# Performance work log

Measured on AMD Instinct MI355X. Metric: run time of the kernel, lower is better.

The kernel has to match this reference:

```python
import jax, jax.numpy as jnp
import numpy as np

SCALE = 10000.0
EPS = 1e-5


def _extract_patches(x):
    # x: [B,28,28] int32 -> [B,28,28,9] (3x3 neighborhoods, zero-padded)
    xp = jnp.pad(x, ((0, 0), (1, 1), (1, 1)))
    ps = [xp[:, i:i + 28, j:j + 28] for i in range(3) for j in range(3)]
    return jnp.stack(ps, axis=-1)


def _bn_eval(x, g, b, m, v):
    inv = g / jnp.sqrt(v + EPS)
    return x * inv[None, :, None, None] + (b - m * inv)[None, :, None, None]


def _maxpool2(x):
    return jax.lax.reduce_window(x, -jnp.inf, jax.lax.max,
                                 (1, 1, 2, 2), (1, 1, 2, 2), 'VALID')


def _conv(x, w, b):
    y = jax.lax.conv_general_dilated(x, w, (1, 1), 'SAME',
                                     dimension_numbers=('NCHW', 'OIHW', 'NCHW'))
    return y + b[None, :, None, None]


def setup_inputs() -> dict:
    key = jax.random.key(0)
    ks = jax.random.split(key, 24)
    B = 1024
    inp = {}
    inp['x_img'] = jax.random.randint(ks[0], (B, 28, 28), 0, 256, dtype=jnp.int32)
    # quantized conv1 weights: round(w * 10000), signed
    inp['y_int'] = jax.random.randint(ks[1], (16, 9), 0, 20001, dtype=jnp.int32) - 10000
    inp['bias1'] = jax.random.normal(ks[2], (16,), jnp.float32)
    for i, (c, kg, kb, km, kv) in enumerate([(16, 3, 4, 5, 6), (32, 7, 8, 9, 10), (64, 11, 12, 13, 14)]):
        j = i + 1
        inp[f'g{j}'] = jax.random.uniform(ks[kg], (c,), jnp.float32, 0.5, 1.5)
        inp[f'b{j}'] = jax.random.normal(ks[kb], (c,), jnp.float32)
        inp[f'm{j}'] = jax.random.normal(ks[km], (c,), jnp.float32)
        inp[f'v{j}'] = jax.random.uniform(ks[kv], (c,), jnp.float32, 0.5, 1.5)
    inp['w2'] = jax.random.normal(ks[15], (32, 16, 3, 3), jnp.float32) * 0.1
    inp['bias2'] = jax.random.normal(ks[16], (32,), jnp.float32)
    inp['w3'] = jax.random.normal(ks[17], (64, 32, 3, 3), jnp.float32) * 0.1
    inp['bias3'] = jax.random.normal(ks[18], (64,), jnp.float32)
    inp['w_fc1'] = jax.random.normal(ks[19], (128, 576), jnp.float32) * 0.05
    inp['b_fc1'] = jax.random.normal(ks[20], (128,), jnp.float32)
    inp['w_fc2'] = jax.random.normal(ks[21], (10, 128), jnp.float32) * 0.1
    inp['b_fc2'] = jax.random.normal(ks[22], (10,), jnp.float32)
    return inp


def reference(x_img, y_int, bias1, g1, b1, m1, v1, w2, bias2, g2, b2, m2, v2,
              w3, bias3, g3, b3, m3, v3, w_fc1, b_fc1, w_fc2, b_fc2):
    # IPFE first conv: exact integer inner product <patch, y>, then /10000 + bias
    patches = _extract_patches(x_img)                      # [B,28,28,9] int32
    ip = jnp.einsum('bhwk,ok->bohw', patches, y_int)       # exact int32 dot
    feat = ip.astype(jnp.float32) / SCALE + bias1[None, :, None, None]  # [B,16,28,28]
    feat = _maxpool2(jax.nn.relu(_bn_eval(feat, g1, b1, m1, v1)))       # [B,16,14,14]
    feat = _maxpool2(jax.nn.relu(_bn_eval(_conv(feat, w2, bias2), g2, b2, m2, v2)))  # [B,32,7,7]
    feat = _maxpool2(jax.nn.relu(_bn_eval(_conv(feat, w3, bias3), g3, b3, m3, v3)))  # [B,64,3,3]
    flat = feat.reshape(feat.shape[0], -1)                 # [B,576]
    h = jax.nn.relu(flat @ w_fc1.T + b_fc1)                # [B,128] (dropout: eval mode)
    return h @ w_fc2.T + b_fc2                             # [B,10]
```

## Files before the change

kernel.cpp:

```cpp
#include <hip/hip_runtime.h>
#include <hip/hip_bf16.h>

#define EPS 1e-5f

typedef __attribute__((ext_vector_type(8))) short bf16x8;
typedef __attribute__((ext_vector_type(4))) float f32x4;
typedef unsigned short ushort_t;
#define MFMA16(a, b, c) __builtin_amdgcn_mfma_f32_16x16x32_bf16(a, b, c, 0, 0, 0)

#define CST_OFF  144
#define W2F_H    1024
#define W3F_H    6144
#define WFC1F_H  24576
#define PREP_ITEMS (368 + 5120 + 18432 + 73728)

__device__ __forceinline__ unsigned short f2bf(float f) {
    unsigned int u = __builtin_bit_cast(unsigned int, f);
    return (unsigned short)((u + 0x7fffu + ((u >> 16) & 1u)) >> 16);
}

__global__ __launch_bounds__(256) void prep_kernel(
    const int* __restrict__ y_int,
    const float* __restrict__ w2, const float* __restrict__ w3,
    const float* __restrict__ wfc1,
    const float* __restrict__ bias1,
    const float* __restrict__ g1, const float* __restrict__ b1,
    const float* __restrict__ m1, const float* __restrict__ v1,
    const float* __restrict__ g2, const float* __restrict__ b2,
    const float* __restrict__ m2, const float* __restrict__ v2,
    const float* __restrict__ bias2,
    const float* __restrict__ g3, const float* __restrict__ b3,
    const float* __restrict__ m3, const float* __restrict__ v3,
    const float* __restrict__ bias3,
    float* __restrict__ ws)
{
    unsigned short* wsh = (unsigned short*)ws;
    int i = blockIdx.x * 256 + threadIdx.x;
    if (i < 144) {
        int k = i >> 4, c = i & 15;
        ws[i] = (float)y_int[c * 9 + k];
    } else if (i < 368) {
        int idx = i - 144;
        if (idx < 16) { int c = idx;
            ws[CST_OFF + idx] = g1[c] * rsqrtf(v1[c] + EPS) * 1e-4f;
        } else if (idx < 32) { int c = idx - 16;
            float inv = g1[c] * rsqrtf(v1[c] + EPS);
            ws[CST_OFF + idx] = bias1[c] * inv + b1[c] - m1[c] * inv;
        } else if (idx < 64) { int c = idx - 32;
            ws[CST_OFF + idx] = g2[c] * rsqrtf(v2[c] + EPS);
        } else if (idx < 96) { int c = idx - 64;
            float inv = g2[c] * rsqrtf(v2[c] + EPS);
            ws[CST_OFF + idx] = bias2[c] * inv + b2[c] - m2[c] * inv;
        } else if (idx < 160) { int c = idx - 96;
            ws[CST_OFF + idx] = g3[c] * rsqrtf(v3[c] + EPS);
        } else { int c = idx - 160;
            float inv = g3[c] * rsqrtf(v3[c] + EPS);
            ws[CST_OFF + idx] = bias3[c] * inv + b3[c] - m3[c] * inv;
        }
    } else {
        int e = i - 368;
        if (e < 5120) {
            int m = e / 2560, r = e % 2560, s = r >> 9, l = (r >> 3) & 63, j = e & 7;
            int kl  = ((l >> 4) << 3) + j;
            int tap = 2 * s + (kl >> 4), ci = kl & 15;
            int ch  = m * 16 + (l & 15);
            float v = (tap < 9) ? w2[ch * 144 + ci * 9 + tap] : 0.f;
            wsh[W2F_H + e] = f2bf(v);
        } else if (e < 5120 + 18432) {
            int e3 = e - 5120;
            int mt = e3 / 4608, r = e3 % 4608, ks = r >> 9, l = (r >> 3) & 63, j = e3 & 7;
            int ch = mt * 16 + (l & 15), ci = ((l >> 4) << 3) + j;
            wsh[W3F_H + e3] = f2bf(w3[ch * 288 + ci * 9 + ks]);
        } else {
            int ef = e - 23552;
            int mt = ef / 9216, r = ef % 9216, ks = r >> 9, l = (r >> 3) & 63, j = ef & 7;
            int ch = mt * 16 + (l & 15), k = ks * 32 + ((l >> 4) << 3) + j;
            wsh[WFC1F_H + ef] = f2bf(wfc1[ch * 576 + k]);
        }
    }
}

__global__ __launch_bounds__(256, 4) void fused_cnn(
    const int* __restrict__ x_img,
    const float* __restrict__ ws,
    const float* __restrict__ bfc1,
    const float* __restrict__ wfc2, const float* __restrict__ bfc2,
    float* __restrict__ out)
{
    const int tid  = threadIdx.x;
    const int lane = tid & 63;
    const int wv   = __builtin_amdgcn_readfirstlane(tid >> 6);
    const int img  = blockIdx.x;
    const unsigned short* wsh = (const unsigned short*)ws;

    __shared__ __align__(16) float s_img[900];
    __shared__ __align__(16) char  s_f1[8192];
    __shared__ __align__(16) char  s_f2[5184];
    ushort_t* FLAT = (ushort_t*)s_f1;
    float*    H    = (float*)(s_f1 + 1152);

    const int* xp = x_img + img * 784;
    for (int i = tid; i < 900; i += 256) {
        int r = i / 30, c = i - r * 30;
        float v = 0.f;
        if (r >= 1 && r <= 28 && c >= 1 && c <= 28)
            v = (float)xp[(r - 1) * 28 + (c - 1)];
        s_img[i] = v;
    }
    {
        uint4 z = make_uint4(0u, 0u, 0u, 0u);
        for (int i = tid; i < 512; i += 256) ((uint4*)s_f1)[i] = z;
        for (int i = tid; i < 324; i += 256) ((uint4*)s_f2)[i] = z;
    }
    __syncthreads();

    if (tid < 196) {
        int ph = tid / 14, pw = tid - (tid / 14) * 14;
        float acc[16][4];
        #pragma unroll
        for (int c = 0; c < 16; c++) {
            acc[c][0] = 0.f; acc[c][1] = 0.f; acc[c][2] = 0.f; acc[c][3] = 0.f;
        }
        const float* imgq = s_img + ph * 60 + pw * 2;
        #pragma unroll
        for (int k = 0; k < 9; k++) {
            const float* ip = imgq + (k / 3) * 30 + (k % 3);
            float x0 = ip[0], x1 = ip[1], x2 = ip[30], x3 = ip[31];
            const float4* yw = (const float4*)(ws + k * 16);
            float4 wA = yw[0], wB = yw[1], wC = yw[2], wD = yw[3];
            float wr[16] = {wA.x, wA.y, wA.z, wA.w, wB.x, wB.y, wB.z, wB.w,
                            wC.x, wC.y, wC.z, wC.w, wD.x, wD.y, wD.z, wD.w};
            #pragma unroll
            for (int c = 0; c < 16; c++) {
                float w = wr[c];
                acc[c][0] += w * x0; acc[c][1] += w * x1;
                acc[c][2] += w * x2; acc[c][3] += w * x3;
            }
        }
        unsigned int pk[8];
        #pragma unroll
        for (int c = 0; c < 16; c += 2) {
            float mx0 = fmaxf(fmaxf(acc[c][0], acc[c][1]), fmaxf(acc[c][2], acc[c][3]));
            float r0  = fmaxf(mx0 * ws[CST_OFF + c] + ws[CST_OFF + 16 + c], 0.f);
            float mx1 = fmaxf(fmaxf(acc[c+1][0], acc[c+1][1]), fmaxf(acc[c+1][2], acc[c+1][3]));
            float r1  = fmaxf(mx1 * ws[CST_OFF + c + 1] + ws[CST_OFF + 16 + c + 1], 0.f);
            pk[c >> 1] = (unsigned int)f2bf(r0) | ((unsigned int)f2bf(r1) << 16);
        }
        int pos = (ph + 1) * 16 + (pw + 1);
        *(uint4*)(s_f1 + pos * 16)        = make_uint4(pk[0], pk[1], pk[2], pk[3]);
        *(uint4*)(s_f1 + 4096 + pos * 16) = make_uint4(pk[4], pk[5], pk[6], pk[7]);
    }
    __syncthreads();

    {
        const int x = lane & 15, g = lane >> 4;
        const int t = g >> 1, c0 = g & 1;
        bf16x8 A2[2][5];
        #pragma unroll
        for (int m = 0; m < 2; m++)
            #pragma unroll
            for (int s = 0; s < 5; s++)
                A2[m][s] = *(const bf16x8*)(const void*)(wsh + W2F_H + ((m * 5 + s) * 64 + lane) * 8);
        int voff[5];
        #pragma unroll
        for (int s = 0; s < 5; s++) {
            int tap = 2 * s + t;
            int dy = (tap < 9) ? tap / 3 : 0, dx = (tap < 9) ? tap % 3 : 0;
            voff[s] = c0 * 4096 + (dy * 16 + x + dx) * 16;
        }
        float a2v[2][4], c2v[2][4];
        #pragma unroll
        for (int m = 0; m < 2; m++)
            #pragma unroll
            for (int r = 0; r < 4; r++) {
                int ch = m * 16 + g * 4 + r;
                a2v[m][r] = ws[CST_OFF + 32 + ch];
                c2v[m][r] = ws[CST_OFF + 64 + ch];
            }
        for (int p = wv; p < 7; p += 4) {
            const char* bp = s_f1 + p * 512;
            bf16x8 B0[5], B1[5];
            #pragma unroll
            for (int s = 0; s < 5; s++) {
                B0[s] = *(const bf16x8*)(const void*)(bp + voff[s]);
                B1[s] = *(const bf16x8*)(const void*)(bp + 256 + voff[s]);
            }
            #pragma unroll
            for (int m = 0; m < 2; m++) {
                f32x4 a0 = {0.f, 0.f, 0.f, 0.f}, a1 = {0.f, 0.f, 0.f, 0.f};
                #pragma unroll
                for (int s = 0; s < 5; s++) {
                    a0 = MFMA16(A2[m][s], B0[s], a0);
                    a1 = MFMA16(A2[m][s], B1[s], a1);
                }
                float hp[4];
                #pragma unroll
                for (int r = 0; r < 4; r++) {
                    float vp = fmaxf(a0[r], a1[r]);
                    hp[r] = fmaxf(vp, __shfl_xor(vp, 1));
                }
                if (!(x & 1) && x < 14) {
                    int xp2 = x >> 1;
                    int pp  = (p + 1) * 9 + xp2 + 1;
                    int ch0 = m * 16 + g * 4;
                    unsigned int lo = (unsigned int)f2bf(fmaxf(hp[0] * a2v[m][0] + c2v[m][0], 0.f)) |
                                      ((unsigned int)f2bf(fmaxf(hp[1] * a2v[m][1] + c2v[m][1], 0.f)) << 16);
                    unsigned int hi = (unsigned int)f2bf(fmaxf(hp[2] * a2v[m][2] + c2v[m][2], 0.f)) |
                                      ((unsigned int)f2bf(fmaxf(hp[3] * a2v[m][3] + c2v[m][3], 0.f)) << 16);
                    *(uint2*)(s_f2 + (ch0 >> 3) * 1296 + pp * 16 + (ch0 & 7) * 2) = make_uint2(lo, hi);
                }
            }
        }
    }
    __syncthreads();

    {
        const int mt = wv;
        bf16x8 A3[9];
        #pragma unroll
        for (int ks = 0; ks < 9; ks++)
            A3[ks] = *(const bf16x8*)(const void*)(wsh + W3F_H + ((mt * 9 + ks) * 64 + lane) * 8);
        const int x8 = lane & 7, ry = (lane >> 3) & 1, qg = lane >> 4;
        int voff3[9];
        #pragma unroll
        for (int ks = 0; ks < 9; ks++) {
            int dy = ks / 3, dx = ks % 3;
            voff3[ks] = qg * 1296 + ((ry + dy) * 9 + x8 + dx) * 16;
        }
        float a3v[4], c3v[4];
        #pragma unroll
        for (int r = 0; r < 4; r++) {
            int ch = mt * 16 + qg * 4 + r;
            a3v[r] = ws[CST_OFF + 96 + ch];
            c3v[r] = ws[CST_OFF + 160 + ch];
        }
        #pragma unroll
        for (int t = 0; t < 3; t++) {
            bf16x8 bb[9];
            #pragma unroll
            for (int ks = 0; ks < 9; ks++)
                bb[ks] = *(const bf16x8*)(const void*)(s_f2 + t * 288 + voff3[ks]);
            f32x4 acc = {0.f, 0.f, 0.f, 0.f};
            #pragma unroll
            for (int ks = 0; ks < 9; ks++)
                acc = MFMA16(A3[ks], bb[ks], acc);
            float hp[4];
            #pragma unroll
            for (int r = 0; r < 4; r++) {
                float vp = fmaxf(acc[r], __shfl_xor(acc[r], 8));
                hp[r] = fmaxf(vp, __shfl_xor(vp, 1));
            }
            if (ry == 0 && !(x8 & 1) && x8 < 6) {
                int xp3 = x8 >> 1;
                int ch0 = mt * 16 + qg * 4;
                #pragma unroll
                for (int r = 0; r < 4; r++) {
                    float v = fmaxf(hp[r] * a3v[r] + c3v[r], 0.f);
                    FLAT[(ch0 + r) * 9 + t * 3 + xp3] = f2bf(v);
                }
            }
        }
    }
    __syncthreads();

    {
        const int g = lane >> 4;
        bf16x8 BB[18];
        #pragma unroll
        for (int ks = 0; ks < 18; ks++)
            BB[ks] = *(const bf16x8*)(const void*)(FLAT + ks * 32 + g * 8);
        #pragma unroll
        for (int mi = 0; mi < 2; mi++) {
            int mt = wv + mi * 4;
            f32x4 acc = {0.f, 0.f, 0.f, 0.f};
            #pragma unroll
            for (int ks = 0; ks < 18; ks++) {
                bf16x8 a = *(const bf16x8*)(const void*)(wsh + WFC1F_H + ((mt * 18 + ks) * 64 + lane) * 8);
                acc = MFMA16(a, BB[ks], acc);
            }
            if ((lane & 15) == 0) {
                int ch0 = mt * 16 + g * 4;
                #pragma unroll
                for (int r = 0; r < 4; r++)
                    H[ch0 + r] = fmaxf(acc[r] + bfc1[ch0 + r], 0.f);
            }
        }
    }
    __syncthreads();

    if (tid < 160) {
        int o = tid / 16, l = tid & 15;
        float a = 0.f;
        #pragma unroll
        for (int k = l; k < 128; k += 16)
            a += H[k] * wfc2[o * 128 + k];
        a += __shfl_xor(a, 8);
        a += __shfl_xor(a, 4);
        a += __shfl_xor(a, 2);
        a += __shfl_xor(a, 1);
        if (l == 0) out[img * 10 + o] = a + bfc2[o];
    }
}

extern "C" void kernel_launch(void* const* d_in, const int* in_sizes, int n_in,
                              void* d_out, int out_size, void* d_ws, size_t ws_size,
                              hipStream_t stream) {
    float* ws = (float*)d_ws;
    prep_kernel<<<(PREP_ITEMS + 255) / 256, 256, 0, stream>>>(
        (const int*)d_in[1],
        (const float*)d_in[15],
        (const float*)d_in[17],
        (const float*)d_in[19],
        (const float*)d_in[2],
        (const float*)d_in[3], (const float*)d_in[4], (const float*)d_in[5], (const float*)d_in[6],
        (const float*)d_in[7], (const float*)d_in[8], (const float*)d_in[9], (const float*)d_in[10],
        (const float*)d_in[16],
        (const float*)d_in[11], (const float*)d_in[12], (const float*)d_in[13], (const float*)d_in[14],
        (const float*)d_in[18],
        ws);
    fused_cnn<<<1024, 256, 0, stream>>>(
        (const int*)d_in[0],
        ws,
        (const float*)d_in[20],
        (const float*)d_in[21], (const float*)d_in[22],
        (float*)d_out);
}
```

Before: 27.42 us.

## Split per-image pipeline into three independent wave slices with halo recompute

Each block now uses three waves, and each wave owns one output row of the 3x3 conv3 map. The wave recomputes the halo rows of conv1 and conv2 it needs in private LDS, which removes the block-wide barriers between stages. FC1 is split by K across waves into partial sums that are reduced after one barrier. The fc1 weight prep is permuted to match the new position-major flatten. This trades redundant conv1/conv2 halo work and reloading all conv3 weights per wave for fewer syncs and more independent wave progress.

Result: slower. 45.45 us (+65.8%).

```diff
diff --git a/kernel.cpp b/kernel.cpp
--- a/kernel.cpp
+++ b/kernel.cpp
@@ -74,13 +74,15 @@
         } else {
             int ef = e - 23552;
             int mt = ef / 9216, r = ef % 9216, ks = r >> 9, l = (r >> 3) & 63, j = ef & 7;
-            int ch = mt * 16 + (l & 15), k = ks * 32 + ((l >> 4) << 3) + j;
-            wsh[WFC1F_H + ef] = f2bf(wfc1[ch * 576 + k]);
+            int ch = mt * 16 + (l & 15);
+            int kp = ks * 32 + ((l >> 4) << 3) + j;
+            int ci = kp & 63, pos = kp >> 6;
+            wsh[WFC1F_H + ef] = f2bf(wfc1[ch * 576 + ci * 9 + pos]);
         }
     }
 }
 
-__global__ __launch_bounds__(256, 4) void fused_cnn(
+__global__ __launch_bounds__(192, 3) void fused_cnn(
     const int* __restrict__ x_img,
     const float* __restrict__ ws,
     const float* __restrict__ bfc1,
@@ -93,35 +95,43 @@
     const int img  = blockIdx.x;
     const unsigned short* wsh = (const unsigned short*)ws;
 
-    __shared__ __align__(16) float s_img[900];
-    __shared__ __align__(16) char  s_f1[8192];
-    __shared__ __align__(16) char  s_f2[5184];
-    ushort_t* FLAT = (ushort_t*)s_f1;
-    float*    H    = (float*)(s_f1 + 1152);
-
-    const int* xp = x_img + img * 784;
-    for (int i = tid; i < 900; i += 256) {
-        int r = i / 30, c = i - r * 30;
-        float v = 0.f;
-        if (r >= 1 && r <= 28 && c >= 1 && c <= 28)
-            v = (float)xp[(r - 1) * 28 + (c - 1)];
-        s_img[i] = v;
-    }
+    __shared__ __align__(16) char s_all[32928];
+    char*     W    = s_all + wv * 10080;
+    float*    IMG  = (float*)W;
+    char*     F1w  = W + 2640;
+    char*     F2w  = W + 7760;
+    ushort_t* FLAT = (ushort_t*)(s_all + 30240);
+    float*    Hp   = (float*)(s_all + 31392);
+
+    const int F0  = (wv == 0) ? 0 : (wv == 1) ? 2 : 6;
+    const int I0  = (wv == 0) ? 0 : (wv == 1) ? 2 : 10;
+    const int PR0 = (wv == 0) ? 0 : (wv == 1) ? 1 : 5;
+    const int NQ  = (wv == 0) ? 98 : (wv == 1) ? 140 : 126;
+    const int PX0 = (wv == 0) ? 0 : (wv == 1) ? 1 : 9;
+    const int NPX = (wv == 0) ? 15 : (wv == 1) ? 22 : 19;
+    const int PS  = (wv == 0) ? 0 : (wv == 1) ? 1 : 3;
+    const int PC  = (wv == 0) ? 3 : 4;
+    const int LR0 = (wv == 0) ? -1 : (wv == 1) ? 1 : 3;
+
     {
         uint4 z = make_uint4(0u, 0u, 0u, 0u);
-        for (int i = tid; i < 512; i += 256) ((uint4*)s_f1)[i] = z;
-        for (int i = tid; i < 324; i += 256) ((uint4*)s_f2)[i] = z;
-    }
-    __syncthreads();
-
-    if (tid < 196) {
-        int ph = tid / 14, pw = tid - (tid / 14) * 14;
+        uint4* zp = (uint4*)W;
+        for (int j = lane; j < 630; j += 64) zp[j] = z;
+    }
+    const int* xp = x_img + img * 784;
+    for (int j = lane; j < NPX * 28; j += 64) {
+        int rr = j / 28, cc = j - rr * 28;
+        IMG[(PX0 + rr + 1 - I0) * 30 + 1 + cc] = (float)xp[(PX0 + rr) * 28 + cc];
+    }
+
+    for (int q = lane; q < NQ; q += 64) {
+        int pr = PR0 + q / 14, pw = q % 14;
         float acc[16][4];
         #pragma unroll
         for (int c = 0; c < 16; c++) {
             acc[c][0] = 0.f; acc[c][1] = 0.f; acc[c][2] = 0.f; acc[c][3] = 0.f;
         }
-        const float* imgq = s_img + ph * 60 + pw * 2;
+        const float* imgq = IMG + (2 * pr - I0) * 30 + pw * 2;
         #pragma unroll
         for (int k = 0; k < 9; k++) {
             const float* ip = imgq + (k / 3) * 30 + (k % 3);
@@ -146,15 +156,14 @@
             float r1  = fmaxf(mx1 * ws[CST_OFF + c + 1] + ws[CST_OFF + 16 + c + 1], 0.f);
             pk[c >> 1] = (unsigned int)f2bf(r0) | ((unsigned int)f2bf(r1) << 16);
         }
-        int pos = (ph + 1) * 16 + (pw + 1);
-        *(uint4*)(s_f1 + pos * 16)        = make_uint4(pk[0], pk[1], pk[2], pk[3]);
-        *(uint4*)(s_f1 + 4096 + pos * 16) = make_uint4(pk[4], pk[5], pk[6], pk[7]);
-    }
-    __syncthreads();
+        int L = pr + 1 - F0;
+        *(uint4*)(F1w + L * 256 + (pw + 1) * 16)        = make_uint4(pk[0], pk[1], pk[2], pk[3]);
+        *(uint4*)(F1w + 2560 + L * 256 + (pw + 1) * 16) = make_uint4(pk[4], pk[5], pk[6], pk[7]);
+    }
 
     {
         const int x = lane & 15, g = lane >> 4;
-        const int t = g >> 1, c0 = g & 1;
+        const int t2 = g >> 1, c0 = g & 1;
         bf16x8 A2[2][5];
         #pragma unroll
         for (int m = 0; m < 2; m++)
@@ -164,9 +173,9 @@
         int voff[5];
         #pragma unroll
         for (int s = 0; s < 5; s++) {
-            int tap = 2 * s + t;
+            int tap = 2 * s + t2;
             int dy = (tap < 9) ? tap / 3 : 0, dx = (tap < 9) ? tap % 3 : 0;
-            voff[s] = c0 * 4096 + (dy * 16 + x + dx) * 16;
+            voff[s] = c0 * 2560 + (dy * 16 + x + dx) * 16;
         }
         float a2v[2][4], c2v[2][4];
         #pragma unroll
@@ -177,8 +186,9 @@
                 a2v[m][r] = ws[CST_OFF + 32 + ch];
                 c2v[m][r] = ws[CST_OFF + 64 + ch];
             }
-        for (int p = wv; p < 7; p += 4) {
-            const char* bp = s_f1 + p * 512;
+        for (int i = 0; i < PC; i++) {
+            int p = PS + i;
+            const char* bp = F1w + (2 * p - F0) * 256;
             bf16x8 B0[5], B1[5];
             #pragma unroll
             for (int s = 0; s < 5; s++) {
@@ -201,45 +211,32 @@
                 }
                 if (!(x & 1) && x < 14) {
                     int xp2 = x >> 1;
-                    int pp  = (p + 1) * 9 + xp2 + 1;
+                    int lrow = p - LR0;
                     int ch0 = m * 16 + g * 4;
                     unsigned int lo = (unsigned int)f2bf(fmaxf(hp[0] * a2v[m][0] + c2v[m][0], 0.f)) |
                                       ((unsigned int)f2bf(fmaxf(hp[1] * a2v[m][1] + c2v[m][1], 0.f)) << 16);
                     unsigned int hi = (unsigned int)f2bf(fmaxf(hp[2] * a2v[m][2] + c2v[m][2], 0.f)) |
                                       ((unsigned int)f2bf(fmaxf(hp[3] * a2v[m][3] + c2v[m][3], 0.f)) << 16);
-                    *(uint2*)(s_f2 + (ch0 >> 3) * 1296 + pp * 16 + (ch0 & 7) * 2) = make_uint2(lo, hi);
+                    *(uint2*)(F2w + (ch0 >> 3) * 576 + (lrow * 9 + xp2 + 1) * 16 + (ch0 & 7) * 2) = make_uint2(lo, hi);
                 }
             }
         }
     }
-    __syncthreads();
 
     {
-        const int mt = wv;
-        bf16x8 A3[9];
-        #pragma unroll
-        for (int ks = 0; ks < 9; ks++)
-            A3[ks] = *(const bf16x8*)(const void*)(wsh + W3F_H + ((mt * 9 + ks) * 64 + lane) * 8);
         const int x8 = lane & 7, ry = (lane >> 3) & 1, qg = lane >> 4;
-        int voff3[9];
+        bf16x8 bb[9];
         #pragma unroll
         for (int ks = 0; ks < 9; ks++) {
             int dy = ks / 3, dx = ks % 3;
-            voff3[ks] = qg * 1296 + ((ry + dy) * 9 + x8 + dx) * 16;
-        }
-        float a3v[4], c3v[4];
-        #pragma unroll
-        for (int r = 0; r < 4; r++) {
-            int ch = mt * 16 + qg * 4 + r;
-            a3v[r] = ws[CST_OFF + 96 + ch];
-            c3v[r] = ws[CST_OFF + 160 + ch];
-        }
-        #pragma unroll
-        for (int t = 0; t < 3; t++) {
-            bf16x8 bb[9];
+            bb[ks] = *(const bf16x8*)(const void*)(F2w + qg * 576 + ((ry + dy) * 9 + x8 + dx) * 16);
+        }
+        #pragma unroll
+        for (int mt = 0; mt < 4; mt++) {
+            bf16x8 A3[9];
             #pragma unroll
             for (int ks = 0; ks < 9; ks++)
-                bb[ks] = *(const bf16x8*)(const void*)(s_f2 + t * 288 + voff3[ks]);
+                A3[ks] = *(const bf16x8*)(const void*)(wsh + W3F_H + ((mt * 9 + ks) * 64 + lane) * 8);
             f32x4 acc = {0.f, 0.f, 0.f, 0.f};
             #pragma unroll
             for (int ks = 0; ks < 9; ks++)
@@ -255,50 +252,55 @@
                 int ch0 = mt * 16 + qg * 4;
                 #pragma unroll
                 for (int r = 0; r < 4; r++) {
-                    float v = fmaxf(hp[r] * a3v[r] + c3v[r], 0.f);
-                    FLAT[(ch0 + r) * 9 + t * 3 + xp3] = f2bf(v);
+                    float a3 = ws[CST_OFF + 96 + ch0 + r];
+                    float c3 = ws[CST_OFF + 160 + ch0 + r];
+                    float v = fmaxf(hp[r] * a3 + c3, 0.f);
+                    FLAT[(wv * 3 + xp3) * 64 + ch0 + r] = f2bf(v);
                 }
             }
         }
     }
-    __syncthreads();
 
     {
         const int g = lane >> 4;
-        bf16x8 BB[18];
-        #pragma unroll
-        for (int ks = 0; ks < 18; ks++)
-            BB[ks] = *(const bf16x8*)(const void*)(FLAT + ks * 32 + g * 8);
-        #pragma unroll
-        for (int mi = 0; mi < 2; mi++) {
-            int mt = wv + mi * 4;
-            f32x4 acc = {0.f, 0.f, 0.f, 0.f};
-            #pragma unroll
-            for (int ks = 0; ks < 18; ks++) {
-                bf16x8 a = *(const bf16x8*)(const void*)(wsh + WFC1F_H + ((mt * 18 + ks) * 64 + lane) * 8);
-                acc = MFMA16(a, BB[ks], acc);
-            }
-            if ((lane & 15) == 0) {
-                int ch0 = mt * 16 + g * 4;
+        f32x4 acc8[8];
+        #pragma unroll
+        for (int mt = 0; mt < 8; mt++) acc8[mt] = (f32x4){0.f, 0.f, 0.f, 0.f};
+        #pragma unroll
+        for (int mt = 0; mt < 8; mt++) {
+            #pragma unroll
+            for (int ksl = 0; ksl < 6; ksl++) {
+                int ks = wv * 6 + ksl;
+                bf16x8 a  = *(const bf16x8*)(const void*)(wsh + WFC1F_H + ((mt * 18 + ks) * 64 + lane) * 8);
+                bf16x8 bv = *(const bf16x8*)(const void*)(FLAT + ks * 32 + g * 8);
+                acc8[mt] = MFMA16(a, bv, acc8[mt]);
+            }
+        }
+        if ((lane & 15) == 0) {
+            #pragma unroll
+            for (int mt = 0; mt < 8; mt++)
                 #pragma unroll
                 for (int r = 0; r < 4; r++)
-                    H[ch0 + r] = fmaxf(acc[r] + bfc1[ch0 + r], 0.f);
-            }
+                    Hp[wv * 128 + mt * 16 + g * 4 + r] = acc8[mt][r];
         }
     }
     __syncthreads();
 
-    if (tid < 160) {
-        int o = tid / 16, l = tid & 15;
-        float a = 0.f;
-        #pragma unroll
-        for (int k = l; k < 128; k += 16)
-            a += H[k] * wfc2[o * 128 + k];
-        a += __shfl_xor(a, 8);
-        a += __shfl_xor(a, 4);
-        a += __shfl_xor(a, 2);
-        a += __shfl_xor(a, 1);
-        if (l == 0) out[img * 10 + o] = a + bfc2[o];
+    if (wv == 0) {
+        int ch = lane * 2;
+        float h0 = fmaxf(Hp[ch]     + Hp[128 + ch]     + Hp[256 + ch]     + bfc1[ch],     0.f);
+        float h1 = fmaxf(Hp[ch + 1] + Hp[128 + ch + 1] + Hp[256 + ch + 1] + bfc1[ch + 1], 0.f);
+        #pragma unroll
+        for (int o = 0; o < 10; o++) {
+            float a = wfc2[o * 128 + ch] * h0 + wfc2[o * 128 + ch + 1] * h1;
+            a += __shfl_xor(a, 32);
+            a += __shfl_xor(a, 16);
+            a += __shfl_xor(a, 8);
+            a += __shfl_xor(a, 4);
+            a += __shfl_xor(a, 2);
+            a += __shfl_xor(a, 1);
+            if (lane == 0) out[img * 10 + o] = a + bfc2[o];
+        }
     }
 }
 
@@ -318,7 +320,7 @@
         (const float*)d_in[11], (const float*)d_in[12], (const float*)d_in[13], (const float*)d_in[14],
         (const float*)d_in[18],
         ws);
-    fused_cnn<<<1024, 256, 0, stream>>>(
+    fused_cnn<<<1024, 192, 0, stream>>>(
         (const int*)d_in[0],
         ws,
         (const float*)d_in[20],
```

## Split FC1 by K per wave, load image directly, zero only borders

Applied to the files above, without the earlier changes.

Each wave now does FC1 on its own conv3 output-channel slice (K split) instead of waiting for all of FLAT, which removes one block-wide barrier. The per-wave partial sums are combined along with bias and ReLU in the FC2 stage. The FC1 weight layout is padded to 160 entries per wave slice, and conv1 reads its 4x4 pixel neighbourhoods straight from global memory instead of a padded shared image. This drops the s_img stage and another barrier. Only the halo borders of the shared feature buffers are zeroed now, at the cost of more FC1 weight traffic and redundant global pixel loads.

Measured after the change: 27.22 us (median of 2 runs). No clear change (-0.7%).

```diff
diff --git a/kernel.cpp b/kernel.cpp
--- a/kernel.cpp
+++ b/kernel.cpp
@@ -12,7 +12,7 @@
 #define W2F_H    1024
 #define W3F_H    6144
 #define WFC1F_H  24576
-#define PREP_ITEMS (368 + 5120 + 18432 + 73728)
+#define PREP_ITEMS (368 + 5120 + 18432 + 81920)
 
 __device__ __forceinline__ unsigned short f2bf(float f) {
     unsigned int u = __builtin_bit_cast(unsigned int, f);
@@ -73,9 +73,14 @@
             wsh[W3F_H + e3] = f2bf(w3[ch * 288 + ci * 9 + ks]);
         } else {
             int ef = e - 23552;
-            int mt = ef / 9216, r = ef % 9216, ks = r >> 9, l = (r >> 3) & 63, j = ef & 7;
-            int ch = mt * 16 + (l & 15), k = ks * 32 + ((l >> 4) << 3) + j;
-            wsh[WFC1F_H + ef] = f2bf(wfc1[ch * 576 + k]);
+            int mt = ef / 10240, r = ef % 10240;
+            int ks = r >> 9, l = (r >> 3) & 63, j = ef & 7;
+            int ch = mt * 16 + (l & 15);
+            int kp = ks * 32 + ((l >> 4) << 3) + j;
+            int w  = kp / 160, lk = kp - w * 160;
+            float v = 0.f;
+            if (lk < 144) v = wfc1[ch * 576 + (w * 16 + lk / 9) * 9 + (lk % 9)];
+            wsh[WFC1F_H + ef] = f2bf(v);
         }
     }
 }
@@ -93,39 +98,59 @@
     const int img  = blockIdx.x;
     const unsigned short* wsh = (const unsigned short*)ws;
 
-    __shared__ __align__(16) float s_img[900];
-    __shared__ __align__(16) char  s_f1[8192];
-    __shared__ __align__(16) char  s_f2[5184];
+    __shared__ __align__(16) char s_f1[8192];
+    __shared__ __align__(16) char s_f2[5184];
     ushort_t* FLAT = (ushort_t*)s_f1;
-    float*    H    = (float*)(s_f1 + 1152);
-
-    const int* xp = x_img + img * 784;
-    for (int i = tid; i < 900; i += 256) {
-        int r = i / 30, c = i - r * 30;
-        float v = 0.f;
-        if (r >= 1 && r <= 28 && c >= 1 && c <= 28)
-            v = (float)xp[(r - 1) * 28 + (c - 1)];
-        s_img[i] = v;
-    }
+    float*    Hp   = (float*)(s_f1 + 1536);
+
     {
         uint4 z = make_uint4(0u, 0u, 0u, 0u);
-        for (int i = tid; i < 512; i += 256) ((uint4*)s_f1)[i] = z;
-        for (int i = tid; i < 324; i += 256) ((uint4*)s_f2)[i] = z;
-    }
-    __syncthreads();
+        if (tid < 120) {
+            int c0 = tid / 60, b = tid % 60, pos;
+            if (b < 16)      pos = b;
+            else if (b < 32) pos = 240 + (b - 16);
+            else if (b < 46) pos = (b - 31) * 16;
+            else             pos = (b - 45) * 16 + 15;
+            *(uint4*)(s_f1 + c0 * 4096 + pos * 16) = z;
+        } else if (tid < 248) {
+            int zz = tid - 120;
+            int q = zz / 32, b = zz % 32, pos;
+            if (b < 9)       pos = b;
+            else if (b < 18) pos = 72 + (b - 9);
+            else if (b < 25) pos = (b - 17) * 9;
+            else             pos = (b - 24) * 9 + 8;
+            *(uint4*)(s_f2 + q * 1296 + pos * 16) = z;
+        }
+    }
 
     if (tid < 196) {
         int ph = tid / 14, pw = tid - (tid / 14) * 14;
+        const int* xp = x_img + img * 784;
+        int ry0 = 2 * ph - 1, cx0 = 2 * pw - 1;
+        float px[4][4];
+        #pragma unroll
+        for (int dy = 0; dy < 4; dy++) {
+            int ry = ry0 + dy;
+            int ryc = min(max(ry, 0), 27);
+            bool rok = (unsigned)ry < 28u;
+            #pragma unroll
+            for (int dx = 0; dx < 4; dx++) {
+                int cx = cx0 + dx;
+                int cxc = min(max(cx, 0), 27);
+                float v = (float)xp[ryc * 28 + cxc];
+                px[dy][dx] = (rok && (unsigned)cx < 28u) ? v : 0.f;
+            }
+        }
         float acc[16][4];
         #pragma unroll
         for (int c = 0; c < 16; c++) {
             acc[c][0] = 0.f; acc[c][1] = 0.f; acc[c][2] = 0.f; acc[c][3] = 0.f;
         }
-        const float* imgq = s_img + ph * 60 + pw * 2;
         #pragma unroll
         for (int k = 0; k < 9; k++) {
-            const float* ip = imgq + (k / 3) * 30 + (k % 3);
-            float x0 = ip[0], x1 = ip[1], x2 = ip[30], x3 = ip[31];
+            int ty = k / 3, tx = k % 3;
+            float x0 = px[ty][tx],     x1 = px[ty][tx + 1];
+            float x2 = px[ty + 1][tx], x3 = px[ty + 1][tx + 1];
             const float4* yw = (const float4*)(ws + k * 16);
             float4 wA = yw[0], wB = yw[1], wC = yw[2], wD = yw[3];
             float wr[16] = {wA.x, wA.y, wA.z, wA.w, wB.x, wB.y, wB.z, wB.w,
@@ -154,7 +179,7 @@
 
     {
         const int x = lane & 15, g = lane >> 4;
-        const int t = g >> 1, c0 = g & 1;
+        const int t2 = g >> 1, c0 = g & 1;
         bf16x8 A2[2][5];
         #pragma unroll
         for (int m = 0; m < 2; m++)
@@ -164,7 +189,7 @@
         int voff[5];
         #pragma unroll
         for (int s = 0; s < 5; s++) {
-            int tap = 2 * s + t;
+            int tap = 2 * s + t2;
             int dy = (tap < 9) ? tap / 3 : 0, dx = (tap < 9) ? tap % 3 : 0;
             voff[s] = c0 * 4096 + (dy * 16 + x + dx) * 16;
         }
@@ -234,6 +259,7 @@
             a3v[r] = ws[CST_OFF + 96 + ch];
             c3v[r] = ws[CST_OFF + 160 + ch];
         }
+        if (lane < 16) FLAT[wv * 160 + 144 + lane] = 0;
         #pragma unroll
         for (int t = 0; t < 3; t++) {
             bf16x8 bb[9];
@@ -252,37 +278,33 @@
             }
             if (ry == 0 && !(x8 & 1) && x8 < 6) {
                 int xp3 = x8 >> 1;
-                int ch0 = mt * 16 + qg * 4;
                 #pragma unroll
                 for (int r = 0; r < 4; r++) {
                     float v = fmaxf(hp[r] * a3v[r] + c3v[r], 0.f);
-                    FLAT[(ch0 + r) * 9 + t * 3 + xp3] = f2bf(v);
+                    FLAT[wv * 160 + (qg * 4 + r) * 9 + t * 3 + xp3] = f2bf(v);
                 }
             }
         }
-    }
-    __syncthreads();
-
-    {
+
         const int g = lane >> 4;
-        bf16x8 BB[18];
-        #pragma unroll
-        for (int ks = 0; ks < 18; ks++)
-            BB[ks] = *(const bf16x8*)(const void*)(FLAT + ks * 32 + g * 8);
-        #pragma unroll
-        for (int mi = 0; mi < 2; mi++) {
-            int mt = wv + mi * 4;
+        bf16x8 BV[5];
+        #pragma unroll
+        for (int ksl = 0; ksl < 5; ksl++)
+            BV[ksl] = *(const bf16x8*)(const void*)(FLAT + (wv * 5 + ksl) * 32 + g * 8);
+        #pragma unroll
+        for (int mtf = 0; mtf < 8; mtf++) {
             f32x4 acc = {0.f, 0.f, 0.f, 0.f};
             #pragma unroll
-            for (int ks = 0; ks < 18; ks++) {
-                bf16x8 a = *(const bf16x8*)(const void*)(wsh + WFC1F_H + ((mt * 18 + ks) * 64 + lane) * 8);
-                acc = MFMA16(a, BB[ks], acc);
+            for (int ksl = 0; ksl < 5; ksl++) {
+                int ks = wv * 5 + ksl;
+                bf16x8 a = *(const bf16x8*)(const void*)(wsh + WFC1F_H + ((mtf * 20 + ks) * 64 + lane) * 8);
+                acc = MFMA16(a, BV[ksl], acc);
             }
             if ((lane & 15) == 0) {
-                int ch0 = mt * 16 + g * 4;
+                int ch0 = mtf * 16 + g * 4;
                 #pragma unroll
                 for (int r = 0; r < 4; r++)
-                    H[ch0 + r] = fmaxf(acc[r] + bfc1[ch0 + r], 0.f);
+                    Hp[wv * 128 + ch0 + r] = acc[r];
             }
         }
     }
@@ -292,8 +314,11 @@
         int o = tid / 16, l = tid & 15;
         float a = 0.f;
         #pragma unroll
-        for (int k = l; k < 128; k += 16)
-            a += H[k] * wfc2[o * 128 + k];
+        for (int k = l; k < 128; k += 16) {
+            float h = Hp[k] + Hp[128 + k] + Hp[256 + k] + Hp[384 + k] + bfc1[k];
+            h = fmaxf(h, 0.f);
+            a += h * wfc2[o * 128 + k];
+        }
         a += __shfl_xor(a, 8);
         a += __shfl_xor(a, 4);
         a += __shfl_xor(a, 2);
```

## Double block to 512 threads and redistribute per-stage work across eight waves

Applied to the files above, without the earlier changes.

Raises the block size to 512 threads and spreads every stage over more waves. Conv1 now uses two threads per pooled pixel that read the image straight from global memory, dropping the shared image staging and a barrier. Conv2 splits output-channel tiles across waves, conv3 splits row tiles, and fc1 gives one M-tile to each of the eight waves. Only the padding borders are zeroed, in parallel with conv1. This shortens the per-wave serial chain, at the cost of more threads per block and possible register-pressure limits under the new launch bounds.

Result: slower. 30.59 us (+11.6%).

```diff
diff --git a/kernel.cpp b/kernel.cpp
--- a/kernel.cpp
+++ b/kernel.cpp
@@ -80,7 +80,7 @@
     }
 }
 
-__global__ __launch_bounds__(256, 4) void fused_cnn(
+__global__ __launch_bounds__(512, 8) void fused_cnn(
     const int* __restrict__ x_img,
     const float* __restrict__ ws,
     const float* __restrict__ bfc1,
@@ -93,39 +93,58 @@
     const int img  = blockIdx.x;
     const unsigned short* wsh = (const unsigned short*)ws;
 
-    __shared__ __align__(16) float s_img[900];
-    __shared__ __align__(16) char  s_f1[8192];
-    __shared__ __align__(16) char  s_f2[5184];
+    __shared__ __align__(16) char s_f1[8192];
+    __shared__ __align__(16) char s_f2[5184];
     ushort_t* FLAT = (ushort_t*)s_f1;
-    float*    H    = (float*)(s_f1 + 1152);
-
-    const int* xp = x_img + img * 784;
-    for (int i = tid; i < 900; i += 256) {
-        int r = i / 30, c = i - r * 30;
-        float v = 0.f;
-        if (r >= 1 && r <= 28 && c >= 1 && c <= 28)
-            v = (float)xp[(r - 1) * 28 + (c - 1)];
-        s_img[i] = v;
-    }
+    float*    H    = (float*)(s_f1 + 1536);
+
     {
         uint4 z = make_uint4(0u, 0u, 0u, 0u);
-        for (int i = tid; i < 512; i += 256) ((uint4*)s_f1)[i] = z;
-        for (int i = tid; i < 324; i += 256) ((uint4*)s_f2)[i] = z;
-    }
-    __syncthreads();
-
-    if (tid < 196) {
-        int ph = tid / 14, pw = tid - (tid / 14) * 14;
-        float acc[16][4];
-        #pragma unroll
-        for (int c = 0; c < 16; c++) {
-            acc[c][0] = 0.f; acc[c][1] = 0.f; acc[c][2] = 0.f; acc[c][3] = 0.f;
-        }
-        const float* imgq = s_img + ph * 60 + pw * 2;
+        if (tid >= 392 && tid < 512) {
+            int zz = tid - 392;
+            int c0 = zz / 60, b = zz % 60, pos;
+            if (b < 16)      pos = b;
+            else if (b < 32) pos = 240 + (b - 16);
+            else if (b < 46) pos = (b - 31) * 16;
+            else             pos = (b - 45) * 16 + 15;
+            *(uint4*)(s_f1 + c0 * 4096 + pos * 16) = z;
+        } else if (tid >= 264 && tid < 392) {
+            int zz = tid - 264;
+            int q = zz / 32, b = zz % 32, pos;
+            if (b < 9)       pos = b;
+            else if (b < 18) pos = 72 + (b - 9);
+            else if (b < 25) pos = (b - 17) * 9;
+            else             pos = (b - 24) * 9 + 8;
+            *(uint4*)(s_f2 + q * 1296 + pos * 16) = z;
+        }
+    }
+
+    if (tid < 392) {
+        int q = tid >> 1, ry = tid & 1;
+        int ph = q / 14, pw = q - (q / 14) * 14;
+        const int* xp = x_img + img * 784;
+        int ybase = 2 * ph + ry - 1, cx0 = 2 * pw - 1;
+        float px[3][4];
+        #pragma unroll
+        for (int dy = 0; dy < 3; dy++) {
+            int yy = ybase + dy;
+            int yyc = min(max(yy, 0), 27);
+            bool rok = (unsigned)yy < 28u;
+            #pragma unroll
+            for (int dx = 0; dx < 4; dx++) {
+                int cx = cx0 + dx;
+                int cxc = min(max(cx, 0), 27);
+                float v = (float)xp[yyc * 28 + cxc];
+                px[dy][dx] = (rok && (unsigned)cx < 28u) ? v : 0.f;
+            }
+        }
+        float acc[16][2];
+        #pragma unroll
+        for (int c = 0; c < 16; c++) { acc[c][0] = 0.f; acc[c][1] = 0.f; }
         #pragma unroll
         for (int k = 0; k < 9; k++) {
-            const float* ip = imgq + (k / 3) * 30 + (k % 3);
-            float x0 = ip[0], x1 = ip[1], x2 = ip[30], x3 = ip[31];
+            int ty = k / 3, tx = k % 3;
+            float x0 = px[ty][tx], x1 = px[ty][tx + 1];
             const float4* yw = (const float4*)(ws + k * 16);
             float4 wA = yw[0], wB = yw[1], wC = yw[2], wD = yw[3];
             float wr[16] = {wA.x, wA.y, wA.z, wA.w, wB.x, wB.y, wB.z, wB.w,
@@ -134,50 +153,54 @@
             for (int c = 0; c < 16; c++) {
                 float w = wr[c];
                 acc[c][0] += w * x0; acc[c][1] += w * x1;
-                acc[c][2] += w * x2; acc[c][3] += w * x3;
             }
         }
         unsigned int pk[8];
         #pragma unroll
         for (int c = 0; c < 16; c += 2) {
-            float mx0 = fmaxf(fmaxf(acc[c][0], acc[c][1]), fmaxf(acc[c][2], acc[c][3]));
-            float r0  = fmaxf(mx0 * ws[CST_OFF + c] + ws[CST_OFF + 16 + c], 0.f);
-            float mx1 = fmaxf(fmaxf(acc[c+1][0], acc[c+1][1]), fmaxf(acc[c+1][2], acc[c+1][3]));
-            float r1  = fmaxf(mx1 * ws[CST_OFF + c + 1] + ws[CST_OFF + 16 + c + 1], 0.f);
+            float m0 = fmaxf(acc[c][0], acc[c][1]);
+            m0 = fmaxf(m0, __shfl_xor(m0, 1));
+            float r0 = fmaxf(m0 * ws[CST_OFF + c] + ws[CST_OFF + 16 + c], 0.f);
+            float m1 = fmaxf(acc[c+1][0], acc[c+1][1]);
+            m1 = fmaxf(m1, __shfl_xor(m1, 1));
+            float r1 = fmaxf(m1 * ws[CST_OFF + c + 1] + ws[CST_OFF + 16 + c + 1], 0.f);
             pk[c >> 1] = (unsigned int)f2bf(r0) | ((unsigned int)f2bf(r1) << 16);
         }
-        int pos = (ph + 1) * 16 + (pw + 1);
-        *(uint4*)(s_f1 + pos * 16)        = make_uint4(pk[0], pk[1], pk[2], pk[3]);
-        *(uint4*)(s_f1 + 4096 + pos * 16) = make_uint4(pk[4], pk[5], pk[6], pk[7]);
+        if (ry == 0) {
+            int pos = (ph + 1) * 16 + (pw + 1);
+            *(uint4*)(s_f1 + pos * 16)        = make_uint4(pk[0], pk[1], pk[2], pk[3]);
+            *(uint4*)(s_f1 + 4096 + pos * 16) = make_uint4(pk[4], pk[5], pk[6], pk[7]);
+        }
     }
     __syncthreads();
 
     {
+        const int m = wv & 1;
         const int x = lane & 15, g = lane >> 4;
-        const int t = g >> 1, c0 = g & 1;
-        bf16x8 A2[2][5];
-        #pragma unroll
-        for (int m = 0; m < 2; m++)
-            #pragma unroll
-            for (int s = 0; s < 5; s++)
-                A2[m][s] = *(const bf16x8*)(const void*)(wsh + W2F_H + ((m * 5 + s) * 64 + lane) * 8);
+        const int tapb = g >> 1, c0 = g & 1;
+        bf16x8 A2[5];
+        #pragma unroll
+        for (int s = 0; s < 5; s++)
+            A2[s] = *(const bf16x8*)(const void*)(wsh + W2F_H + ((m * 5 + s) * 64 + lane) * 8);
         int voff[5];
         #pragma unroll
         for (int s = 0; s < 5; s++) {
-            int tap = 2 * s + t;
+            int tap = 2 * s + tapb;
             int dy = (tap < 9) ? tap / 3 : 0, dx = (tap < 9) ? tap % 3 : 0;
             voff[s] = c0 * 4096 + (dy * 16 + x + dx) * 16;
         }
-        float a2v[2][4], c2v[2][4];
-        #pragma unroll
-        for (int m = 0; m < 2; m++)
-            #pragma unroll
-            for (int r = 0; r < 4; r++) {
-                int ch = m * 16 + g * 4 + r;
-                a2v[m][r] = ws[CST_OFF + 32 + ch];
-                c2v[m][r] = ws[CST_OFF + 64 + ch];
-            }
-        for (int p = wv; p < 7; p += 4) {
+        float a2v[4], c2v[4];
+        #pragma unroll
+        for (int r = 0; r < 4; r++) {
+            int ch = m * 16 + g * 4 + r;
+            a2v[r] = ws[CST_OFF + 32 + ch];
+            c2v[r] = ws[CST_OFF + 64 + ch];
+        }
+        const int pbase = wv >> 1;
+        #pragma unroll
+        for (int pi = 0; pi < 2; pi++) {
+            int p = pbase + pi * 4;
+            if (p > 6) break;
             const char* bp = s_f1 + p * 512;
             bf16x8 B0[5], B1[5];
             #pragma unroll
@@ -185,37 +208,34 @@
                 B0[s] = *(const bf16x8*)(const void*)(bp + voff[s]);
                 B1[s] = *(const bf16x8*)(const void*)(bp + 256 + voff[s]);
             }
-            #pragma unroll
-            for (int m = 0; m < 2; m++) {
-                f32x4 a0 = {0.f, 0.f, 0.f, 0.f}, a1 = {0.f, 0.f, 0.f, 0.f};
-                #pragma unroll
-                for (int s = 0; s < 5; s++) {
-                    a0 = MFMA16(A2[m][s], B0[s], a0);
-                    a1 = MFMA16(A2[m][s], B1[s], a1);
-                }
-                float hp[4];
-                #pragma unroll
-                for (int r = 0; r < 4; r++) {
-                    float vp = fmaxf(a0[r], a1[r]);
-                    hp[r] = fmaxf(vp, __shfl_xor(vp, 1));
-                }
-                if (!(x & 1) && x < 14) {
-                    int xp2 = x >> 1;
-                    int pp  = (p + 1) * 9 + xp2 + 1;
-                    int ch0 = m * 16 + g * 4;
-                    unsigned int lo = (unsigned int)f2bf(fmaxf(hp[0] * a2v[m][0] + c2v[m][0], 0.f)) |
-                                      ((unsigned int)f2bf(fmaxf(hp[1] * a2v[m][1] + c2v[m][1], 0.f)) << 16);
-                    unsigned int hi = (unsigned int)f2bf(fmaxf(hp[2] * a2v[m][2] + c2v[m][2], 0.f)) |
-                                      ((unsigned int)f2bf(fmaxf(hp[3] * a2v[m][3] + c2v[m][3], 0.f)) << 16);
-                    *(uint2*)(s_f2 + (ch0 >> 3) * 1296 + pp * 16 + (ch0 & 7) * 2) = make_uint2(lo, hi);
-                }
+            f32x4 a0 = {0.f, 0.f, 0.f, 0.f}, a1 = {0.f, 0.f, 0.f, 0.f};
+            #pragma unroll
+            for (int s = 0; s < 5; s++) {
+                a0 = MFMA16(A2[s], B0[s], a0);
+                a1 = MFMA16(A2[s], B1[s], a1);
+            }
+            float hp[4];
+            #pragma unroll
+            for (int r = 0; r < 4; r++) {
+                float vp = fmaxf(a0[r], a1[r]);
+                hp[r] = fmaxf(vp, __shfl_xor(vp, 1));
+            }
+            if (!(x & 1) && x < 14) {
+                int xp2 = x >> 1;
+                int pp  = (p + 1) * 9 + xp2 + 1;
+                int ch0 = m * 16 + g * 4;
+                unsigned int lo = (unsigned int)f2bf(fmaxf(hp[0] * a2v[0] + c2v[0], 0.f)) |
+                                  ((unsigned int)f2bf(fmaxf(hp[1] * a2v[1] + c2v[1], 0.f)) << 16);
+                unsigned int hi = (unsigned int)f2bf(fmaxf(hp[2] * a2v[2] + c2v[2], 0.f)) |
+                                  ((unsigned int)f2bf(fmaxf(hp[3] * a2v[3] + c2v[3], 0.f)) << 16);
+                *(uint2*)(s_f2 + (ch0 >> 3) * 1296 + pp * 16 + (ch0 & 7) * 2) = make_uint2(lo, hi);
             }
         }
     }
     __syncthreads();
 
     {
-        const int mt = wv;
+        const int mt = wv & 3;
         bf16x8 A3[9];
         #pragma unroll
         for (int ks = 0; ks < 9; ks++)
@@ -235,7 +255,9 @@
             c3v[r] = ws[CST_OFF + 160 + ch];
         }
         #pragma unroll
-        for (int t = 0; t < 3; t++) {
+        for (int ti = 0; ti < 2; ti++) {
+            int t = (ti == 0) ? (wv >> 2) : 2;
+            if (ti == 1 && wv >= 4) break;
             bf16x8 bb[9];
             #pragma unroll
             for (int ks = 0; ks < 9; ks++)
@@ -265,25 +287,19 @@
 
     {
         const int g = lane >> 4;
-        bf16x8 BB[18];
-        #pragma unroll
-        for (int ks = 0; ks < 18; ks++)
-            BB[ks] = *(const bf16x8*)(const void*)(FLAT + ks * 32 + g * 8);
-        #pragma unroll
-        for (int mi = 0; mi < 2; mi++) {
-            int mt = wv + mi * 4;
-            f32x4 acc = {0.f, 0.f, 0.f, 0.f};
-            #pragma unroll
-            for (int ks = 0; ks < 18; ks++) {
-                bf16x8 a = *(const bf16x8*)(const void*)(wsh + WFC1F_H + ((mt * 18 + ks) * 64 + lane) * 8);
-                acc = MFMA16(a, BB[ks], acc);
-            }
-            if ((lane & 15) == 0) {
-                int ch0 = mt * 16 + g * 4;
-                #pragma unroll
-                for (int r = 0; r < 4; r++)
-                    H[ch0 + r] = fmaxf(acc[r] + bfc1[ch0 + r], 0.f);
-            }
+        const int mt = wv;
+        f32x4 acc = {0.f, 0.f, 0.f, 0.f};
+        #pragma unroll
+        for (int ks = 0; ks < 18; ks++) {
+            bf16x8 a  = *(const bf16x8*)(const void*)(wsh + WFC1F_H + ((mt * 18 + ks) * 64 + lane) * 8);
+            bf16x8 bv = *(const bf16x8*)(const void*)(FLAT + ks * 32 + g * 8);
+            acc = MFMA16(a, bv, acc);
+        }
+        if ((lane & 15) == 0) {
+            int ch0 = mt * 16 + g * 4;
+            #pragma unroll
+            for (int r = 0; r < 4; r++)
+                H[ch0 + r] = fmaxf(acc[r] + bfc1[ch0 + r], 0.f);
         }
     }
     __syncthreads();
@@ -318,7 +334,7 @@
         (const float*)d_in[11], (const float*)d_in[12], (const float*)d_in[13], (const float*)d_in[14],
         (const float*)d_in[18],
         ws);
-    fused_cnn<<<1024, 256, 0, stream>>>(
+    fused_cnn<<<1024, 512, 0, stream>>>(
         (const int*)d_in[0],
         ws,
         (const float*)d_in[20],
```
